# Kernel tuning notes

Measured on AMD Instinct MI355X. Metric: run time of the kernel, lower is better.

## Reference

```python
import jax, jax.numpy as jnp
import numpy as np

N_NODES = 100000
N_EDGES = 1600000
IN_DIM = 256
HID = 64
OUT_DIM = 1
N_GRAPHS = 100


def setup_inputs() -> dict:
    key = jax.random.key(0)
    ks = jax.random.split(key, 12)
    x = jax.random.normal(ks[0], (N_NODES, IN_DIM), dtype=jnp.float32)
    edge_index = jax.random.randint(ks[1], (2, N_EDGES), 0, N_NODES, dtype=jnp.int64 if jax.config.read('jax_enable_x64') else jnp.int32)
    batch = jnp.sort(jax.random.randint(ks[2], (N_NODES,), 0, N_GRAPHS, dtype=jnp.int32))
    def lin(k, fan_in, fan_out):
        bound = 1.0 / np.sqrt(fan_in)
        kw, kb = jax.random.split(k)
        W = jax.random.uniform(kw, (fan_in, fan_out), minval=-bound, maxval=bound, dtype=jnp.float32)
        b = jax.random.uniform(kb, (fan_out,), minval=-bound, maxval=bound, dtype=jnp.float32)
        return W, b
    W1, b1 = lin(ks[3], IN_DIM, HID)
    W2, b2 = lin(ks[4], HID, HID)
    W3, b3 = lin(ks[5], HID, HID)
    Wl, bl = lin(ks[6], HID, OUT_DIM)
    return {"x": x, "edge_index": edge_index, "batch": batch,
            "W1": W1, "b1": b1, "W2": W2, "b2": b2, "W3": W3, "b3": b3,
            "Wl": Wl, "bl": bl}


def _gcn_layer(h, src, dst, norm, W, b):
    # PyG GCNConv: h' = scatter_add(norm * (h @ W)[src] -> dst) + b
    h = h @ W                                   # [N, F_out]
    msg = h[src] * norm[:, None]                # [E+N, F_out] irregular gather
    agg = jax.ops.segment_sum(msg, dst, num_segments=N_NODES)
    return agg + b


def reference(x, edge_index, batch, W1, b1, W2, b2, W3, b3, Wl, bl):
    # add self loops (static shape) as GCNConv does by default
    loops = jnp.arange(N_NODES, dtype=edge_index.dtype)
    src = jnp.concatenate([edge_index[0], loops])  # [E+N]
    dst = jnp.concatenate([edge_index[1], loops])  # [E+N]
    # symmetric normalization: deg over targets incl. self loops
    deg = jax.ops.segment_sum(jnp.ones_like(dst, dtype=x.dtype), dst, num_segments=N_NODES)
    dinv = jnp.where(deg > 0, jax.lax.rsqrt(deg), 0.0)
    norm = dinv[src] * dinv[dst]                # [E+N]

    h = jax.nn.relu(_gcn_layer(x, src, dst, norm, W1, b1))
    h = jax.nn.relu(_gcn_layer(h, src, dst, norm, W2, b2))
    h = _gcn_layer(h, src, dst, norm, W3, b3)   # last conv: no relu

    # global_add_pool over graphs; dropout is identity at inference
    pooled = jax.ops.segment_sum(h, batch, num_segments=N_GRAPHS)  # [G, HID]
    return pooled @ Wl + bl                     # [G, 1]
```

## Files before the change

### kernel.cpp

```cpp
#include <hip/hip_runtime.h>

#define N_NODES 100000
#define N_EDGES 1600000
#define IN_DIM 256
#define HID 64
#define N_GRAPHS 100
#define NPART 256
#define PSTRIDE 128
#define BSHIFT 8
#define NBUCK 391
#define CHUNK 4096

typedef __attribute__((ext_vector_type(8))) short short8;
typedef __attribute__((ext_vector_type(8))) unsigned short us8;
typedef __attribute__((ext_vector_type(4))) float floatx4;

__device__ __forceinline__ unsigned short f2b(float f) {
    unsigned int u = __float_as_uint(f);
    unsigned int r = (u + 0x7FFFu + ((u >> 16) & 1u)) >> 16;
    return (unsigned short)r;
}
__device__ __forceinline__ float b2f(unsigned short b) {
    return __uint_as_float(((unsigned int)b) << 16);
}


__global__ void k_wprep(const float* __restrict__ W1, const float* __restrict__ W2,
                        const float* __restrict__ W3, const float* __restrict__ Wl,
                        const float* __restrict__ b3,
                        unsigned short* __restrict__ wt1, unsigned short* __restrict__ wt2,
                        float* __restrict__ w3l) {
    int i = blockIdx.x * 256 + threadIdx.x;
    if (i < IN_DIM * HID) {
        int k = i >> 6, n = i & 63;
        wt1[n * IN_DIM + k] = f2b(W1[i]);
    }
    if (i < HID * HID) {
        int k = i >> 6, n = i & 63;
        wt2[n * HID + k] = f2b(W2[i]);
    }
    if (blockIdx.x == 0) {
        int t = threadIdx.x;
        if (t < HID) {
            float s = 0.f;
            for (int n = 0; n < HID; ++n) s += W3[t * HID + n] * Wl[n];
            w3l[t] = s;
        } else if (t == HID) {
            float s = 0.f;
            for (int n = 0; n < HID; ++n) s += b3[n] * Wl[n];
            w3l[HID] = s;
        }
    }
}


__global__ void k_zero_misc(int* __restrict__ bcount, float* __restrict__ partial) {
    int i = blockIdx.x * 256 + threadIdx.x;
    if (i < NBUCK) bcount[i] = 0;
    if (i < NPART * PSTRIDE) partial[i] = 0.f;
}

__global__ __launch_bounds__(256) void k_bhist(const int* __restrict__ dst,
                                               int* __restrict__ bcount) {
    __shared__ int lc[NBUCK];
    int t = threadIdx.x;
    for (int b = t; b < NBUCK; b += 256) lc[b] = 0;
    __syncthreads();
    int base = blockIdx.x * CHUNK;
#pragma unroll
    for (int i = 0; i < 16; ++i) {
        int e = base + i * 256 + t;
        if (e < N_EDGES) atomicAdd(&lc[dst[e] >> BSHIFT], 1);
    }
    __syncthreads();
    for (int b = t; b < NBUCK; b += 256)
        if (lc[b]) atomicAdd(&bcount[b], lc[b]);
}

__global__ void k_bscan(const int* __restrict__ bcount, int* __restrict__ bstart,
                        int* __restrict__ bfill) {
    __shared__ int s[512];
    int t = threadIdx.x;
    int v = (t < NBUCK) ? bcount[t] : 0;
    s[t] = v; __syncthreads();
    for (int off = 1; off < 512; off <<= 1) {
        int u = 0;
        if (t >= off) u = s[t - off];
        __syncthreads();
        s[t] += u;
        __syncthreads();
    }
    if (t < NBUCK) { int st = s[t] - v; bstart[t] = st; bfill[t] = st; }
    if (t == 0) bstart[NBUCK] = N_EDGES;
}

__global__ __launch_bounds__(256) void k_bscatter(const int* __restrict__ src,
                                                  const int* __restrict__ dst,
                                                  int* __restrict__ bfill,
                                                  int* __restrict__ ebuck) {
    __shared__ int lc[NBUCK];
    __shared__ int lb[NBUCK];
    int t = threadIdx.x;
    for (int b = t; b < NBUCK; b += 256) lc[b] = 0;
    __syncthreads();
    int base = blockIdx.x * CHUNK;
    int pk[16], bk[16], rk[16];
#pragma unroll
    for (int i = 0; i < 16; ++i) {
        int e = base + i * 256 + t;
        rk[i] = -1;
        if (e < N_EDGES) {
            int s = src[e], d = dst[e];
            bk[i] = d >> BSHIFT;
            pk[i] = (s << BSHIFT) | (d & 255);
            rk[i] = atomicAdd(&lc[bk[i]], 1);
        }
    }
    __syncthreads();
    for (int b = t; b < NBUCK; b += 256)
        lb[b] = lc[b] ? atomicAdd(&bfill[b], lc[b]) : 0;
    __syncthreads();
#pragma unroll
    for (int i = 0; i < 16; ++i)
        if (rk[i] >= 0) ebuck[lb[bk[i]] + rk[i]] = pk[i];
}

__global__ __launch_bounds__(256) void k_degscan(const int* __restrict__ bstart,
                                                 const int* __restrict__ ebuck,
                                                 int* __restrict__ deg,
                                                 float* __restrict__ dinv,
                                                 int* __restrict__ bsum) {
    __shared__ int ld[256];
    __shared__ int rs[256];
    int b = blockIdx.x, t = threadIdx.x;
    ld[t] = 1;
    __syncthreads();
    int s = bstart[b], e = bstart[b + 1];
    for (int j = s + t; j < e; j += 256) atomicAdd(&ld[ebuck[j] & 255], 1);
    __syncthreads();
    int node = (b << BSHIFT) + t;
    int d = ld[t];
    if (node < N_NODES) {
        deg[node] = d;
        dinv[node] = rsqrtf((float)d);
    }
    rs[t] = (node < N_NODES) ? d - 1 : 0;
    __syncthreads();
    for (int off = 128; off; off >>= 1) {
        if (t < off) rs[t] += rs[t + off];
        __syncthreads();
    }
    if (t == 0) bsum[b] = rs[0];
}

__global__ void k_scan2(const int* __restrict__ bsum, int* __restrict__ bscan, int nb) {
    __shared__ int s[512];
    int t = threadIdx.x;
    int v = (t < nb) ? bsum[t] : 0;
    s[t] = v; __syncthreads();
    for (int off = 1; off < 512; off <<= 1) {
        int u = 0;
        if (t >= off) u = s[t - off];
        __syncthreads();
        s[t] += u;
        __syncthreads();
    }
    if (t < nb) bscan[t] = s[t] - v;
}

__global__ __launch_bounds__(256) void k_fill2(const int* __restrict__ bstart,
                                               const int* __restrict__ ebuck,
                                               const int* __restrict__ deg,
                                               const int* __restrict__ bscan,
                                               int* __restrict__ rowptr,
                                               int* __restrict__ col) {
    __shared__ int s[256];
    __shared__ int lf[256];
    int b = blockIdx.x, t = threadIdx.x;
    int node = (b << BSHIFT) + t;
    int c = (node < N_NODES) ? deg[node] - 1 : 0;
    s[t] = c; __syncthreads();
    for (int off = 1; off < 256; off <<= 1) {
        int u = 0;
        if (t >= off) u = s[t - off];
        __syncthreads();
        s[t] += u;
        __syncthreads();
    }
    int pos = bscan[b] + s[t] - c;
    if (node < N_NODES) rowptr[node] = pos;
    lf[t] = pos;
    __syncthreads();
    int st = bstart[b], e = bstart[b + 1];
    for (int j = st + t; j < e; j += 256) {
        int v = ebuck[j];
        int p = atomicAdd(&lf[v & 255], 1);
        col[p] = v >> BSHIFT;
    }
}


__global__ __launch_bounds__(256) void k_gemm1(const float* __restrict__ X,
                                               const unsigned short* __restrict__ Wt,
                                               const float* __restrict__ dinv,
                                               unsigned short* __restrict__ Tb) {
    __shared__ unsigned short Wb[64][264];
    const int t = threadIdx.x;
    const int lane = t & 63, wv = t >> 6;
    const int fl = lane & 15, quad = lane >> 4;
    const int r0 = blockIdx.x * 64;

    for (int g = t; g < 64 * 32; g += 256) {
        int n = g >> 5, kc8 = g & 31;
        *(us8*)&Wb[n][kc8 * 8] = *(const us8*)(Wt + n * IN_DIM + kc8 * 8);
    }

    const int arow = r0 + wv * 16 + fl;
    const bool valid = arow < N_NODES;
    const float* xp = X + (size_t)(valid ? arow : 0) * IN_DIM;

    floatx4 acc[4];
#pragma unroll
    for (int j = 0; j < 4; ++j) acc[j] = (floatx4){0.f, 0.f, 0.f, 0.f};

    __syncthreads();

#pragma unroll
    for (int kc = 0; kc < IN_DIM; kc += 32) {
        float4 x0 = make_float4(0.f, 0.f, 0.f, 0.f);
        float4 x1 = make_float4(0.f, 0.f, 0.f, 0.f);
        if (valid) {
            x0 = *(const float4*)(xp + kc + quad * 8);
            x1 = *(const float4*)(xp + kc + quad * 8 + 4);
        }
        short8 a;
        a[0] = (short)f2b(x0.x); a[1] = (short)f2b(x0.y);
        a[2] = (short)f2b(x0.z); a[3] = (short)f2b(x0.w);
        a[4] = (short)f2b(x1.x); a[5] = (short)f2b(x1.y);
        a[6] = (short)f2b(x1.z); a[7] = (short)f2b(x1.w);
#pragma unroll
        for (int ct = 0; ct < 4; ++ct) {
            short8 b = *(const short8*)&Wb[ct * 16 + fl][kc + quad * 8];
            acc[ct] = __builtin_amdgcn_mfma_f32_16x16x32_bf16(a, b, acc[ct], 0, 0, 0);
        }
    }

    int rbase = r0 + wv * 16 + quad * 4;
#pragma unroll
    for (int r = 0; r < 4; ++r) {
        int row = rbase + r;
        if (row < N_NODES) {
            float di = dinv[row];
#pragma unroll
            for (int ct = 0; ct < 4; ++ct)
                Tb[(size_t)row * HID + ct * 16 + fl] = f2b(di * acc[ct][r]);
        }
    }
}


__global__ __launch_bounds__(256) void k_gemm2(const unsigned short* __restrict__ Xin,
                                               const unsigned short* __restrict__ Wt,
                                               const float* __restrict__ dinv,
                                               unsigned short* __restrict__ Tb) {
    __shared__ unsigned short Wb[64][72];
    const int t = threadIdx.x;
    const int lane = t & 63, wv = t >> 6;
    const int fl = lane & 15, quad = lane >> 4;
    const int r0 = blockIdx.x * 64;

    for (int g = t; g < 64 * 8; g += 256) {
        int n = g >> 3, kc8 = g & 7;
        *(us8*)&Wb[n][kc8 * 8] = *(const us8*)(Wt + n * HID + kc8 * 8);
    }

    const int arow = r0 + wv * 16 + fl;
    const bool valid = arow < N_NODES;
    const unsigned short* xp = Xin + (size_t)(valid ? arow : 0) * HID;

    floatx4 acc[4];
#pragma unroll
    for (int j = 0; j < 4; ++j) acc[j] = (floatx4){0.f, 0.f, 0.f, 0.f};

    __syncthreads();

#pragma unroll
    for (int kc = 0; kc < HID; kc += 32) {
        short8 a = (short8){0, 0, 0, 0, 0, 0, 0, 0};
        if (valid) a = *(const short8*)(xp + kc + quad * 8);
#pragma unroll
        for (int ct = 0; ct < 4; ++ct) {
            short8 b = *(const short8*)&Wb[ct * 16 + fl][kc + quad * 8];
            acc[ct] = __builtin_amdgcn_mfma_f32_16x16x32_bf16(a, b, acc[ct], 0, 0, 0);
        }
    }

    int rbase = r0 + wv * 16 + quad * 4;
#pragma unroll
    for (int r = 0; r < 4; ++r) {
        int row = rbase + r;
        if (row < N_NODES) {
            float di = dinv[row];
#pragma unroll
            for (int ct = 0; ct < 4; ++ct)
                Tb[(size_t)row * HID + ct * 16 + fl] = f2b(di * acc[ct][r]);
        }
    }
}


__global__ __launch_bounds__(256) void k_agg(const unsigned short* __restrict__ Tb,
                                             const int* __restrict__ rowptr,
                                             const int* __restrict__ deg,
                                             const float* __restrict__ dinv,
                                             const int* __restrict__ col,
                                             const float* __restrict__ bias,
                                             unsigned short* __restrict__ Hb) {
    int lane = threadIdx.x & 63;
    int node = blockIdx.x * 4 + (threadIdx.x >> 6);
    int grp = lane >> 3, fl = lane & 7;
    int e = __builtin_amdgcn_readfirstlane(rowptr[node]);
    int end = e + __builtin_amdgcn_readfirstlane(deg[node]) - 1;
    float a0 = 0.f, a1 = 0.f, a2 = 0.f, a3 = 0.f;
    float a4 = 0.f, a5 = 0.f, a6 = 0.f, a7 = 0.f;
    for (; e + 8 <= end; e += 8) {
        int s = col[e + grp];
        us8 tv = *(const us8*)(Tb + (size_t)s * HID + fl * 8);
        a0 += b2f(tv[0]); a1 += b2f(tv[1]); a2 += b2f(tv[2]); a3 += b2f(tv[3]);
        a4 += b2f(tv[4]); a5 += b2f(tv[5]); a6 += b2f(tv[6]); a7 += b2f(tv[7]);
    }
    if (e + grp < end) {
        int s = col[e + grp];
        us8 tv = *(const us8*)(Tb + (size_t)s * HID + fl * 8);
        a0 += b2f(tv[0]); a1 += b2f(tv[1]); a2 += b2f(tv[2]); a3 += b2f(tv[3]);
        a4 += b2f(tv[4]); a5 += b2f(tv[5]); a6 += b2f(tv[6]); a7 += b2f(tv[7]);
    }
    a0 += __shfl_xor(a0, 8);  a1 += __shfl_xor(a1, 8);
    a2 += __shfl_xor(a2, 8);  a3 += __shfl_xor(a3, 8);
    a4 += __shfl_xor(a4, 8);  a5 += __shfl_xor(a5, 8);
    a6 += __shfl_xor(a6, 8);  a7 += __shfl_xor(a7, 8);
    a0 += __shfl_xor(a0, 16); a1 += __shfl_xor(a1, 16);
    a2 += __shfl_xor(a2, 16); a3 += __shfl_xor(a3, 16);
    a4 += __shfl_xor(a4, 16); a5 += __shfl_xor(a5, 16);
    a6 += __shfl_xor(a6, 16); a7 += __shfl_xor(a7, 16);
    a0 += __shfl_xor(a0, 32); a1 += __shfl_xor(a1, 32);
    a2 += __shfl_xor(a2, 32); a3 += __shfl_xor(a3, 32);
    a4 += __shfl_xor(a4, 32); a5 += __shfl_xor(a5, 32);
    a6 += __shfl_xor(a6, 32); a7 += __shfl_xor(a7, 32);
    us8 sv = *(const us8*)(Tb + (size_t)node * HID + fl * 8);
    a0 += b2f(sv[0]); a1 += b2f(sv[1]); a2 += b2f(sv[2]); a3 += b2f(sv[3]);
    a4 += b2f(sv[4]); a5 += b2f(sv[5]); a6 += b2f(sv[6]); a7 += b2f(sv[7]);
    float di = dinv[node];
    float4 b0 = *(const float4*)(bias + fl * 8);
    float4 b1v = *(const float4*)(bias + fl * 8 + 4);
    a0 = fmaxf(fmaf(di, a0, b0.x), 0.f);
    a1 = fmaxf(fmaf(di, a1, b0.y), 0.f);
    a2 = fmaxf(fmaf(di, a2, b0.z), 0.f);
    a3 = fmaxf(fmaf(di, a3, b0.w), 0.f);
    a4 = fmaxf(fmaf(di, a4, b1v.x), 0.f);
    a5 = fmaxf(fmaf(di, a5, b1v.y), 0.f);
    a6 = fmaxf(fmaf(di, a6, b1v.z), 0.f);
    a7 = fmaxf(fmaf(di, a7, b1v.w), 0.f);
    if (grp == 0) {
        us8 o;
        o[0] = f2b(a0); o[1] = f2b(a1); o[2] = f2b(a2); o[3] = f2b(a3);
        o[4] = f2b(a4); o[5] = f2b(a5); o[6] = f2b(a6); o[7] = f2b(a7);
        *(us8*)(Hb + (size_t)node * HID + fl * 8) = o;
    }
}


__global__ __launch_bounds__(256) void k_gemv3(const unsigned short* __restrict__ Hb,
                                               const float* __restrict__ w3l,
                                               const float* __restrict__ dinv,
                                               float* __restrict__ z) {
    int t = threadIdx.x;
    int lane = t & 63, wv = t >> 6;
    int nd = lane >> 3, fl = lane & 7;
    int row = blockIdx.x * 32 + wv * 8 + nd;
    if (row >= N_NODES) return;
    us8 hv = *(const us8*)(Hb + (size_t)row * HID + fl * 8);
    float4 w0 = *(const float4*)(w3l + fl * 8);
    float4 w1 = *(const float4*)(w3l + fl * 8 + 4);
    float s = b2f(hv[0]) * w0.x + b2f(hv[1]) * w0.y + b2f(hv[2]) * w0.z +
              b2f(hv[3]) * w0.w + b2f(hv[4]) * w1.x + b2f(hv[5]) * w1.y +
              b2f(hv[6]) * w1.z + b2f(hv[7]) * w1.w;
    s += __shfl_xor(s, 1);
    s += __shfl_xor(s, 2);
    s += __shfl_xor(s, 4);
    if (fl == 0) z[row] = dinv[row] * s;
}

__global__ __launch_bounds__(256) void k_aggpool_s(const float* __restrict__ z,
                                                   const int* __restrict__ rowptr,
                                                   const int* __restrict__ deg,
                                                   const float* __restrict__ dinv,
                                                   const int* __restrict__ col,
                                                   const float* __restrict__ w3l,
                                                   const int* __restrict__ batch,
                                                   float* __restrict__ partial) {
    int i = blockIdx.x * 256 + threadIdx.x;
    if (i >= N_NODES) return;
    int e = rowptr[i];
    int end = e + deg[i] - 1;
    float s0 = z[i], s1 = 0.f, s2 = 0.f, s3 = 0.f;
    for (; e + 4 <= end; e += 4) {
        s0 += z[col[e]];
        s1 += z[col[e + 1]];
        s2 += z[col[e + 2]];
        s3 += z[col[e + 3]];
    }
    for (; e < end; ++e) s0 += z[col[e]];
    float s = w3l[HID] + dinv[i] * (s0 + s1 + s2 + s3);
    atomicAdd(&partial[(blockIdx.x & (NPART - 1)) * PSTRIDE + batch[i]], s);
}

__global__ void k_pool_reduce(const float* __restrict__ partial,
                              const float* __restrict__ bl,
                              float* __restrict__ out) {
    int g = threadIdx.x;
    if (g >= N_GRAPHS) return;
    float s = bl[0];
    for (int p = 0; p < NPART; ++p) s += partial[p * PSTRIDE + g];
    out[g] = s;
}

extern "C" void kernel_launch(void* const* d_in, const int* in_sizes, int n_in,
                              void* d_out, int out_size, void* d_ws, size_t ws_size,
                              hipStream_t stream) {
    const float* x     = (const float*)d_in[0];
    const int*   ei    = (const int*)d_in[1];
    const int*   batch = (const int*)d_in[2];
    const float* W1    = (const float*)d_in[3];
    const float* b1    = (const float*)d_in[4];
    const float* W2    = (const float*)d_in[5];
    const float* b2    = (const float*)d_in[6];
    const float* W3    = (const float*)d_in[7];
    const float* b3    = (const float*)d_in[8];
    const float* Wl    = (const float*)d_in[9];
    const float* bl    = (const float*)d_in[10];
    float* out = (float*)d_out;

    char* p = (char*)d_ws;
    unsigned short* tb = (unsigned short*)p; p += (size_t)N_NODES * HID * 2;
    unsigned short* hB = (unsigned short*)p; p += (size_t)N_NODES * HID * 2;
    int*   col     = (int*)p;   p += (size_t)(N_EDGES + 16) * 4;
    int*   ebuck   = (int*)p;   p += (size_t)N_EDGES * 4;
    int*   deg     = (int*)p;   p += (size_t)N_NODES * 4;
    float* dinv    = (float*)p; p += (size_t)N_NODES * 4;
    int*   rowptr  = (int*)p;   p += (size_t)N_NODES * 4;
    float* z       = (float*)p; p += (size_t)N_NODES * 4;
    int*   bcount  = (int*)p;   p += (NBUCK + 1) * 4;
    int*   bstart  = (int*)p;   p += (NBUCK + 1) * 4;
    int*   bfill   = (int*)p;   p += (NBUCK + 1) * 4;
    int*   bsum    = (int*)p;   p += 512 * 4;
    int*   bscan   = (int*)p;   p += 512 * 4;
    float* partial = (float*)p; p += (size_t)NPART * PSTRIDE * 4;
    unsigned short* wt1 = (unsigned short*)p; p += (size_t)IN_DIM * HID * 2;
    unsigned short* wt2 = (unsigned short*)p; p += (size_t)HID * HID * 2;
    float* w3l     = (float*)p; p += 128 * 4;

    const int* src  = ei;
    const int* dstp = ei + N_EDGES;

    const int nb = (N_NODES + 255) / 256;
    const int cb = (N_EDGES + CHUNK - 1) / CHUNK;
    const int gemm_blocks = (N_NODES + 63) / 64;
    const int node_wave_blocks = (N_NODES + 3) / 4;

    k_wprep<<<(IN_DIM * HID + 255) / 256, 256, 0, stream>>>(W1, W2, W3, Wl, b3,
                                                            wt1, wt2, w3l);
    k_zero_misc<<<(NPART * PSTRIDE + 255) / 256, 256, 0, stream>>>(bcount, partial);
    k_bhist<<<cb, 256, 0, stream>>>(dstp, bcount);
    k_bscan<<<1, 512, 0, stream>>>(bcount, bstart, bfill);
    k_bscatter<<<cb, 256, 0, stream>>>(src, dstp, bfill, ebuck);
    k_degscan<<<NBUCK, 256, 0, stream>>>(bstart, ebuck, deg, dinv, bsum);
    k_scan2<<<1, 512, 0, stream>>>(bsum, bscan, nb);
    k_fill2<<<NBUCK, 256, 0, stream>>>(bstart, ebuck, deg, bscan, rowptr, col);

    k_gemm1<<<gemm_blocks, 256, 0, stream>>>(x, wt1, dinv, tb);
    k_agg<<<node_wave_blocks, 256, 0, stream>>>(tb, rowptr, deg, dinv, col, b1, hB);
    k_gemm2<<<gemm_blocks, 256, 0, stream>>>(hB, wt2, dinv, tb);
    k_agg<<<node_wave_blocks, 256, 0, stream>>>(tb, rowptr, deg, dinv, col, b2, hB);

    k_gemv3<<<(N_NODES + 31) / 32, 256, 0, stream>>>(hB, w3l, dinv, z);
    k_aggpool_s<<<nb, 256, 0, stream>>>(z, rowptr, deg, dinv, col, w3l, batch, partial);

    k_pool_reduce<<<1, 128, 0, stream>>>(partial, bl, out);
}
```

Measured before the change: 386.6 us.

## Fuse CSR build into one persistent kernel with grid barriers; fuse agg with gemv3

Merges the six graph-preprocessing kernels (histogram, scan, scatter, degree, scan, fill) into a single 391-block kernel that uses software grid barriers, which removes several launch gaps and small single-block scans. Folds the zeroing into the weight-prep kernel. Fuses the layer-2 aggregation with the layer-3 GEMV so the 64-wide hidden state is never written back. Parallelizes the pool reduction across one block per graph with a transposed partial layout. The grid barrier assumes all 391 blocks are co-resident, which risks deadlock if they are not.

```diff
diff --git a/kernel.cpp b/kernel.cpp
--- a/kernel.cpp
+++ b/kernel.cpp
@@ -5,8 +5,6 @@
 #define IN_DIM 256
 #define HID 64
 #define N_GRAPHS 100
-#define NPART 256
-#define PSTRIDE 128
 #define BSHIFT 8
 #define NBUCK 391
 #define CHUNK 4096
@@ -25,11 +23,13 @@
 }
 
 
-__global__ void k_wprep(const float* __restrict__ W1, const float* __restrict__ W2,
-                        const float* __restrict__ W3, const float* __restrict__ Wl,
-                        const float* __restrict__ b3,
-                        unsigned short* __restrict__ wt1, unsigned short* __restrict__ wt2,
-                        float* __restrict__ w3l) {
+__global__ void k_prep(const float* __restrict__ W1, const float* __restrict__ W2,
+                       const float* __restrict__ W3, const float* __restrict__ Wl,
+                       const float* __restrict__ b3,
+                       unsigned short* __restrict__ wt1, unsigned short* __restrict__ wt2,
+                       float* __restrict__ w3l,
+                       int* __restrict__ bcount, int* __restrict__ bfillrel,
+                       float* __restrict__ partial, int* __restrict__ bar) {
     int i = blockIdx.x * 256 + threadIdx.x;
     if (i < IN_DIM * HID) {
         int k = i >> 6, n = i & 63;
@@ -39,6 +39,9 @@
         int k = i >> 6, n = i & 63;
         wt2[n * HID + k] = f2b(W2[i]);
     }
+    if (i < NBUCK) { bcount[i] = 0; bfillrel[i] = 0; }
+    if (i < N_GRAPHS * 256) partial[i] = 0.f;
+    if (i < 8) bar[i] = 0;
     if (blockIdx.x == 0) {
         int t = threadIdx.x;
         if (t < HID) {
@@ -54,148 +57,139 @@
 }
 
 
-__global__ void k_zero_misc(int* __restrict__ bcount, float* __restrict__ partial) {
-    int i = blockIdx.x * 256 + threadIdx.x;
-    if (i < NBUCK) bcount[i] = 0;
-    if (i < NPART * PSTRIDE) partial[i] = 0.f;
-}
-
-__global__ __launch_bounds__(256) void k_bhist(const int* __restrict__ dst,
-                                               int* __restrict__ bcount) {
+__device__ __forceinline__ void grid_bar(int* cnt) {
+    __syncthreads();
+    if (threadIdx.x == 0) {
+        __threadfence();
+        atomicAdd(cnt, 1);
+        while (__hip_atomic_load(cnt, __ATOMIC_RELAXED, __HIP_MEMORY_SCOPE_AGENT) < NBUCK)
+            __builtin_amdgcn_s_sleep(2);
+        __threadfence();
+    }
+    __syncthreads();
+}
+
+__device__ __forceinline__ int* scan512(int* sA, int* sB, int t) {
+    int* A = sA;
+    int* B = sB;
+    for (int off = 1; off < 512; off <<= 1) {
+        B[t] = A[t] + ((t >= off) ? A[t - off] : 0);
+        B[t + 256] = A[t + 256] + A[t + 256 - off];
+        __syncthreads();
+        int* tmp = A; A = B; B = tmp;
+    }
+    return A;
+}
+
+__global__ __launch_bounds__(256) void k_setup(const int* __restrict__ src,
+                                               const int* __restrict__ dstp,
+                                               int* __restrict__ bcount,
+                                               int* __restrict__ bfillrel,
+                                               int* __restrict__ ebuck,
+                                               int* __restrict__ deg,
+                                               float* __restrict__ dinv,
+                                               int* __restrict__ bsum,
+                                               int* __restrict__ rowptr,
+                                               int* __restrict__ col,
+                                               int* __restrict__ bar) {
     __shared__ int lc[NBUCK];
-    int t = threadIdx.x;
-    for (int b = t; b < NBUCK; b += 256) lc[b] = 0;
-    __syncthreads();
-    int base = blockIdx.x * CHUNK;
-#pragma unroll
-    for (int i = 0; i < 16; ++i) {
-        int e = base + i * 256 + t;
-        if (e < N_EDGES) atomicAdd(&lc[dst[e] >> BSHIFT], 1);
-    }
-    __syncthreads();
-    for (int b = t; b < NBUCK; b += 256)
-        if (lc[b]) atomicAdd(&bcount[b], lc[b]);
-}
-
-__global__ void k_bscan(const int* __restrict__ bcount, int* __restrict__ bstart,
-                        int* __restrict__ bfill) {
-    __shared__ int s[512];
-    int t = threadIdx.x;
-    int v = (t < NBUCK) ? bcount[t] : 0;
-    s[t] = v; __syncthreads();
-    for (int off = 1; off < 512; off <<= 1) {
-        int u = 0;
-        if (t >= off) u = s[t - off];
-        __syncthreads();
-        s[t] += u;
-        __syncthreads();
-    }
-    if (t < NBUCK) { int st = s[t] - v; bstart[t] = st; bfill[t] = st; }
-    if (t == 0) bstart[NBUCK] = N_EDGES;
-}
-
-__global__ __launch_bounds__(256) void k_bscatter(const int* __restrict__ src,
-                                                  const int* __restrict__ dst,
-                                                  int* __restrict__ bfill,
-                                                  int* __restrict__ ebuck) {
-    __shared__ int lc[NBUCK];
-    __shared__ int lb[NBUCK];
-    int t = threadIdx.x;
-    for (int b = t; b < NBUCK; b += 256) lc[b] = 0;
-    __syncthreads();
-    int base = blockIdx.x * CHUNK;
+    __shared__ int ebst[NBUCK + 1];
+    __shared__ int sA[512];
+    __shared__ int sB[512];
+    __shared__ int ld[256];
+    __shared__ int lf[256];
+    const int b = blockIdx.x, t = threadIdx.x;
+
+    for (int i = t; i < NBUCK; i += 256) lc[i] = 0;
+    __syncthreads();
+    const int base = b * CHUNK;
     int pk[16], bk[16], rk[16];
 #pragma unroll
     for (int i = 0; i < 16; ++i) {
         int e = base + i * 256 + t;
         rk[i] = -1;
         if (e < N_EDGES) {
-            int s = src[e], d = dst[e];
+            int s = src[e], d = dstp[e];
             bk[i] = d >> BSHIFT;
             pk[i] = (s << BSHIFT) | (d & 255);
             rk[i] = atomicAdd(&lc[bk[i]], 1);
         }
     }
     __syncthreads();
-    for (int b = t; b < NBUCK; b += 256)
-        lb[b] = lc[b] ? atomicAdd(&bfill[b], lc[b]) : 0;
+    for (int i = t; i < NBUCK; i += 256)
+        if (lc[i]) atomicAdd(&bcount[i], lc[i]);
+
+    grid_bar(bar + 0);
+
+    {
+        int v0 = (t < NBUCK) ? bcount[t] : 0;
+        int v1 = (t + 256 < NBUCK) ? bcount[t + 256] : 0;
+        sA[t] = v0;
+        sA[t + 256] = v1;
+        __syncthreads();
+        int* A = scan512(sA, sB, t);
+        if (t < NBUCK) ebst[t] = A[t] - v0;
+        if (t + 256 < NBUCK) ebst[t + 256] = A[t + 256] - v1;
+        if (t == 0) ebst[NBUCK] = N_EDGES;
+        __syncthreads();
+    }
+
+    for (int i = t; i < NBUCK; i += 256)
+        lc[i] = lc[i] ? (ebst[i] + atomicAdd(&bfillrel[i], lc[i])) : 0;
     __syncthreads();
 #pragma unroll
     for (int i = 0; i < 16; ++i)
-        if (rk[i] >= 0) ebuck[lb[bk[i]] + rk[i]] = pk[i];
-}
-
-__global__ __launch_bounds__(256) void k_degscan(const int* __restrict__ bstart,
-                                                 const int* __restrict__ ebuck,
-                                                 int* __restrict__ deg,
-                                                 float* __restrict__ dinv,
-                                                 int* __restrict__ bsum) {
-    __shared__ int ld[256];
-    __shared__ int rs[256];
-    int b = blockIdx.x, t = threadIdx.x;
+        if (rk[i] >= 0) ebuck[lc[bk[i]] + rk[i]] = pk[i];
+
+    grid_bar(bar + 1);
+
+    const int bs = ebst[b], be = ebst[b + 1];
     ld[t] = 1;
     __syncthreads();
-    int s = bstart[b], e = bstart[b + 1];
-    for (int j = s + t; j < e; j += 256) atomicAdd(&ld[ebuck[j] & 255], 1);
-    __syncthreads();
-    int node = (b << BSHIFT) + t;
-    int d = ld[t];
+    for (int j = bs + t; j < be; j += 256) atomicAdd(&ld[ebuck[j] & 255], 1);
+    __syncthreads();
+    const int node = (b << BSHIFT) + t;
+    const int dg = ld[t];
     if (node < N_NODES) {
-        deg[node] = d;
-        dinv[node] = rsqrtf((float)d);
-    }
-    rs[t] = (node < N_NODES) ? d - 1 : 0;
+        deg[node] = dg;
+        dinv[node] = rsqrtf((float)dg);
+    }
+    sA[t] = (node < N_NODES) ? dg - 1 : 0;
     __syncthreads();
     for (int off = 128; off; off >>= 1) {
-        if (t < off) rs[t] += rs[t + off];
-        __syncthreads();
-    }
-    if (t == 0) bsum[b] = rs[0];
-}
-
-__global__ void k_scan2(const int* __restrict__ bsum, int* __restrict__ bscan, int nb) {
-    __shared__ int s[512];
-    int t = threadIdx.x;
-    int v = (t < nb) ? bsum[t] : 0;
-    s[t] = v; __syncthreads();
-    for (int off = 1; off < 512; off <<= 1) {
-        int u = 0;
-        if (t >= off) u = s[t - off];
-        __syncthreads();
-        s[t] += u;
-        __syncthreads();
-    }
-    if (t < nb) bscan[t] = s[t] - v;
-}
-
-__global__ __launch_bounds__(256) void k_fill2(const int* __restrict__ bstart,
-                                               const int* __restrict__ ebuck,
-                                               const int* __restrict__ deg,
-                                               const int* __restrict__ bscan,
-                                               int* __restrict__ rowptr,
-                                               int* __restrict__ col) {
-    __shared__ int s[256];
-    __shared__ int lf[256];
-    int b = blockIdx.x, t = threadIdx.x;
-    int node = (b << BSHIFT) + t;
-    int c = (node < N_NODES) ? deg[node] - 1 : 0;
-    s[t] = c; __syncthreads();
-    for (int off = 1; off < 256; off <<= 1) {
-        int u = 0;
-        if (t >= off) u = s[t - off];
-        __syncthreads();
-        s[t] += u;
-        __syncthreads();
-    }
-    int pos = bscan[b] + s[t] - c;
-    if (node < N_NODES) rowptr[node] = pos;
-    lf[t] = pos;
-    __syncthreads();
-    int st = bstart[b], e = bstart[b + 1];
-    for (int j = st + t; j < e; j += 256) {
-        int v = ebuck[j];
-        int p = atomicAdd(&lf[v & 255], 1);
-        col[p] = v >> BSHIFT;
+        if (t < off) sA[t] += sA[t + off];
+        __syncthreads();
+    }
+    if (t == 0) bsum[b] = sA[0];
+
+    grid_bar(bar + 2);
+
+    {
+        sA[t] = (t < NBUCK) ? bsum[t] : 0;
+        sA[t + 256] = (t + 256 < NBUCK) ? bsum[t + 256] : 0;
+        __syncthreads();
+        int* A = scan512(sA, sB, t);
+        const int off_b = (b > 0) ? A[b - 1] : 0;
+        __syncthreads();
+        int c = (node < N_NODES) ? dg - 1 : 0;
+        sA[t] = c;
+        __syncthreads();
+        for (int off = 1; off < 256; off <<= 1) {
+            int u = 0;
+            if (t >= off) u = sA[t - off];
+            __syncthreads();
+            sA[t] += u;
+            __syncthreads();
+        }
+        const int pos = off_b + sA[t] - c;
+        if (node < N_NODES) rowptr[node] = pos;
+        lf[t] = pos;
+        __syncthreads();
+        for (int j = bs + t; j < be; j += 256) {
+            int v = ebuck[j];
+            int p = atomicAdd(&lf[v & 255], 1);
+            col[p] = v >> BSHIFT;
+        }
     }
 }
 
@@ -370,25 +364,67 @@
 }
 
 
-__global__ __launch_bounds__(256) void k_gemv3(const unsigned short* __restrict__ Hb,
+__global__ __launch_bounds__(256) void k_agg_z(const unsigned short* __restrict__ Tb,
+                                               const int* __restrict__ rowptr,
+                                               const int* __restrict__ deg,
+                                               const float* __restrict__ dinv,
+                                               const int* __restrict__ col,
+                                               const float* __restrict__ bias,
                                                const float* __restrict__ w3l,
-                                               const float* __restrict__ dinv,
                                                float* __restrict__ z) {
-    int t = threadIdx.x;
-    int lane = t & 63, wv = t >> 6;
-    int nd = lane >> 3, fl = lane & 7;
-    int row = blockIdx.x * 32 + wv * 8 + nd;
-    if (row >= N_NODES) return;
-    us8 hv = *(const us8*)(Hb + (size_t)row * HID + fl * 8);
+    int lane = threadIdx.x & 63;
+    int node = blockIdx.x * 4 + (threadIdx.x >> 6);
+    int grp = lane >> 3, fl = lane & 7;
+    int e = __builtin_amdgcn_readfirstlane(rowptr[node]);
+    int end = e + __builtin_amdgcn_readfirstlane(deg[node]) - 1;
+    float a0 = 0.f, a1 = 0.f, a2 = 0.f, a3 = 0.f;
+    float a4 = 0.f, a5 = 0.f, a6 = 0.f, a7 = 0.f;
+    for (; e + 8 <= end; e += 8) {
+        int s = col[e + grp];
+        us8 tv = *(const us8*)(Tb + (size_t)s * HID + fl * 8);
+        a0 += b2f(tv[0]); a1 += b2f(tv[1]); a2 += b2f(tv[2]); a3 += b2f(tv[3]);
+        a4 += b2f(tv[4]); a5 += b2f(tv[5]); a6 += b2f(tv[6]); a7 += b2f(tv[7]);
+    }
+    if (e + grp < end) {
+        int s = col[e + grp];
+        us8 tv = *(const us8*)(Tb + (size_t)s * HID + fl * 8);
+        a0 += b2f(tv[0]); a1 += b2f(tv[1]); a2 += b2f(tv[2]); a3 += b2f(tv[3]);
+        a4 += b2f(tv[4]); a5 += b2f(tv[5]); a6 += b2f(tv[6]); a7 += b2f(tv[7]);
+    }
+    a0 += __shfl_xor(a0, 8);  a1 += __shfl_xor(a1, 8);
+    a2 += __shfl_xor(a2, 8);  a3 += __shfl_xor(a3, 8);
+    a4 += __shfl_xor(a4, 8);  a5 += __shfl_xor(a5, 8);
+    a6 += __shfl_xor(a6, 8);  a7 += __shfl_xor(a7, 8);
+    a0 += __shfl_xor(a0, 16); a1 += __shfl_xor(a1, 16);
+    a2 += __shfl_xor(a2, 16); a3 += __shfl_xor(a3, 16);
+    a4 += __shfl_xor(a4, 16); a5 += __shfl_xor(a5, 16);
+    a6 += __shfl_xor(a6, 16); a7 += __shfl_xor(a7, 16);
+    a0 += __shfl_xor(a0, 32); a1 += __shfl_xor(a1, 32);
+    a2 += __shfl_xor(a2, 32); a3 += __shfl_xor(a3, 32);
+    a4 += __shfl_xor(a4, 32); a5 += __shfl_xor(a5, 32);
+    a6 += __shfl_xor(a6, 32); a7 += __shfl_xor(a7, 32);
+    us8 sv = *(const us8*)(Tb + (size_t)node * HID + fl * 8);
+    a0 += b2f(sv[0]); a1 += b2f(sv[1]); a2 += b2f(sv[2]); a3 += b2f(sv[3]);
+    a4 += b2f(sv[4]); a5 += b2f(sv[5]); a6 += b2f(sv[6]); a7 += b2f(sv[7]);
+    float di = dinv[node];
+    float4 b0 = *(const float4*)(bias + fl * 8);
+    float4 b1v = *(const float4*)(bias + fl * 8 + 4);
+    a0 = fmaxf(fmaf(di, a0, b0.x), 0.f);
+    a1 = fmaxf(fmaf(di, a1, b0.y), 0.f);
+    a2 = fmaxf(fmaf(di, a2, b0.z), 0.f);
+    a3 = fmaxf(fmaf(di, a3, b0.w), 0.f);
+    a4 = fmaxf(fmaf(di, a4, b1v.x), 0.f);
+    a5 = fmaxf(fmaf(di, a5, b1v.y), 0.f);
+    a6 = fmaxf(fmaf(di, a6, b1v.z), 0.f);
+    a7 = fmaxf(fmaf(di, a7, b1v.w), 0.f);
     float4 w0 = *(const float4*)(w3l + fl * 8);
-    float4 w1 = *(const float4*)(w3l + fl * 8 + 4);
-    float s = b2f(hv[0]) * w0.x + b2f(hv[1]) * w0.y + b2f(hv[2]) * w0.z +
-              b2f(hv[3]) * w0.w + b2f(hv[4]) * w1.x + b2f(hv[5]) * w1.y +
-              b2f(hv[6]) * w1.z + b2f(hv[7]) * w1.w;
+    float4 w1v = *(const float4*)(w3l + fl * 8 + 4);
+    float s = a0 * w0.x + a1 * w0.y + a2 * w0.z + a3 * w0.w +
+              a4 * w1v.x + a5 * w1v.y + a6 * w1v.z + a7 * w1v.w;
     s += __shfl_xor(s, 1);
     s += __shfl_xor(s, 2);
     s += __shfl_xor(s, 4);
-    if (fl == 0) z[row] = dinv[row] * s;
+    if (lane == 0) z[node] = di * s;
 }
 
 __global__ __launch_bounds__(256) void k_aggpool_s(const float* __restrict__ z,
@@ -412,17 +448,24 @@
     }
     for (; e < end; ++e) s0 += z[col[e]];
     float s = w3l[HID] + dinv[i] * (s0 + s1 + s2 + s3);
-    atomicAdd(&partial[(blockIdx.x & (NPART - 1)) * PSTRIDE + batch[i]], s);
+    atomicAdd(&partial[batch[i] * 256 + (blockIdx.x & 255)], s);
 }
 
 __global__ void k_pool_reduce(const float* __restrict__ partial,
                               const float* __restrict__ bl,
                               float* __restrict__ out) {
-    int g = threadIdx.x;
-    if (g >= N_GRAPHS) return;
-    float s = bl[0];
-    for (int p = 0; p < NPART; ++p) s += partial[p * PSTRIDE + g];
-    out[g] = s;
+    int g = blockIdx.x, t = threadIdx.x;
+    float s = partial[g * 256 + t];
+    s += __shfl_xor(s, 32);
+    s += __shfl_xor(s, 16);
+    s += __shfl_xor(s, 8);
+    s += __shfl_xor(s, 4);
+    s += __shfl_xor(s, 2);
+    s += __shfl_xor(s, 1);
+    __shared__ float ws[4];
+    if ((t & 63) == 0) ws[t >> 6] = s;
+    __syncthreads();
+    if (t == 0) out[g] = bl[0] + ws[0] + ws[1] + ws[2] + ws[3];
 }
 
 extern "C" void kernel_launch(void* const* d_in, const int* in_sizes, int n_in,
@@ -451,11 +494,10 @@
     int*   rowptr  = (int*)p;   p += (size_t)N_NODES * 4;
     float* z       = (float*)p; p += (size_t)N_NODES * 4;
     int*   bcount  = (int*)p;   p += (NBUCK + 1) * 4;
-    int*   bstart  = (int*)p;   p += (NBUCK + 1) * 4;
-    int*   bfill   = (int*)p;   p += (NBUCK + 1) * 4;
+    int*   bfillr  = (int*)p;   p += (NBUCK + 1) * 4;
     int*   bsum    = (int*)p;   p += 512 * 4;
-    int*   bscan   = (int*)p;   p += 512 * 4;
-    float* partial = (float*)p; p += (size_t)NPART * PSTRIDE * 4;
+    int*   bar     = (int*)p;   p += 16 * 4;
+    float* partial = (float*)p; p += (size_t)N_GRAPHS * 256 * 4;
     unsigned short* wt1 = (unsigned short*)p; p += (size_t)IN_DIM * HID * 2;
     unsigned short* wt2 = (unsigned short*)p; p += (size_t)HID * HID * 2;
     float* w3l     = (float*)p; p += 128 * 4;
@@ -464,27 +506,19 @@
     const int* dstp = ei + N_EDGES;
 
     const int nb = (N_NODES + 255) / 256;
-    const int cb = (N_EDGES + CHUNK - 1) / CHUNK;
     const int gemm_blocks = (N_NODES + 63) / 64;
     const int node_wave_blocks = (N_NODES + 3) / 4;
 
-    k_wprep<<<(IN_DIM * HID + 255) / 256, 256, 0, stream>>>(W1, W2, W3, Wl, b3,
-                                                            wt1, wt2, w3l);
-    k_zero_misc<<<(NPART * PSTRIDE + 255) / 256, 256, 0, stream>>>(bcount, partial);
-    k_bhist<<<cb, 256, 0, stream>>>(dstp, bcount);
-    k_bscan<<<1, 512, 0, stream>>>(bcount, bstart, bfill);
-    k_bscatter<<<cb, 256, 0, stream>>>(src, dstp, bfill, ebuck);
-    k_degscan<<<NBUCK, 256, 0, stream>>>(bstart, ebuck, deg, dinv, bsum);
-    k_scan2<<<1, 512, 0, stream>>>(bsum, bscan, nb);
-    k_fill2<<<NBUCK, 256, 0, stream>>>(bstart, ebuck, deg, bscan, rowptr, col);
+    k_prep<<<128, 256, 0, stream>>>(W1, W2, W3, Wl, b3, wt1, wt2, w3l,
+                                    bcount, bfillr, partial, bar);
+    k_setup<<<NBUCK, 256, 0, stream>>>(src, dstp, bcount, bfillr, ebuck,
+                                       deg, dinv, bsum, rowptr, col, bar);
 
     k_gemm1<<<gemm_blocks, 256, 0, stream>>>(x, wt1, dinv, tb);
     k_agg<<<node_wave_blocks, 256, 0, stream>>>(tb, rowptr, deg, dinv, col, b1, hB);
     k_gemm2<<<gemm_blocks, 256, 0, stream>>>(hB, wt2, dinv, tb);
-    k_agg<<<node_wave_blocks, 256, 0, stream>>>(tb, rowptr, deg, dinv, col, b2, hB);
-
-    k_gemv3<<<(N_NODES + 31) / 32, 256, 0, stream>>>(hB, w3l, dinv, z);
+    k_agg_z<<<node_wave_blocks, 256, 0, stream>>>(tb, rowptr, deg, dinv, col, b2, w3l, z);
+
     k_aggpool_s<<<nb, 256, 0, stream>>>(z, rowptr, deg, dinv, col, w3l, batch, partial);
-
-    k_pool_reduce<<<1, 128, 0, stream>>>(partial, bl, out);
-}
+    k_pool_reduce<<<N_GRAPHS, 256, 0, stream>>>(partial, bl, out);
+}
```

Measured after the change: 500.4 us. 1.29x slower.
